# Kernel tuning notes

Hardware: AMD Instinct MI355X
Metric: run time of the kernel (lower is better)

## Reference

```python
import jax, jax.numpy as jnp
import numpy as np

GRID = 8          # proto_grid
EPS = 1e-4        # safe_norm eps
TAU = 20.0        # temperature used throughout


def avg_pool(x, k):
    # non-overlapping avg pool, kernel k divides H and W exactly
    S, C, H, W = x.shape
    return x.reshape(S, C, H // k, k, W // k, k).mean(axis=(3, 5))


def safe_norm(x, axis):
    n = jnp.sqrt(jnp.sum(x * x, axis=axis, keepdims=True))
    return x / jnp.maximum(n, EPS)


def setup_inputs() -> dict:
    key = jax.random.key(0)
    k1, k2, k3 = jax.random.split(key, 3)
    qry = jax.random.normal(k1, (1, 1, 256, 128, 128), dtype=jnp.float32)
    sup_x = jax.random.normal(k2, (1, 5, 1, 256, 128, 128), dtype=jnp.float32)
    sup_y = jax.random.uniform(k3, (1, 5, 1, 128, 128), dtype=jnp.float32)
    return {"qry": qry, "sup_x": sup_x, "sup_y": sup_y, "thresh": 0}


def reference(qry, sup_x, sup_y, thresh):
    # mode == 'gridconv', use_cross_attn=False, isval=False
    qry = qry[:, 0]          # squeeze(1)        -> [1, 256, 128, 128]
    sup_x = sup_x[0, :, 0]   # squeeze(0,2)      -> [5, 256, 128, 128]
    sup_y = sup_y[0]         # squeeze(0)        -> [5, 1, 128, 128]

    shot, nc, H, W = sup_x.shape
    k = H // GRID

    # grid prototypes: avgpool then [shot, nc, g*g] -> [shot, g*g, nc] -> [shot*g*g, nc]
    n_sup = avg_pool(sup_x, k)
    protos = n_sup.reshape(shot, nc, -1).transpose(0, 2, 1).reshape(-1, nc)
    # selection mask: avg_pool(sup_y) > thresh. sup_y is uniform(0,1) and
    # thresh=0, so every grid cell is selected -> selection is the identity
    # (fixed-shape, jit-safe; matches the torch boolean index exactly here).

    # mean-center then safe L2-normalize (channel dim)
    protos = protos - protos.mean(axis=-1, keepdims=True)
    qryc = qry - qry.mean(axis=1, keepdims=True)
    pro_n = safe_norm(protos, axis=1)        # [npro, nc]
    qry_n = safe_norm(qryc, axis=1)          # [b, nc, h, w]

    # 1x1 conv as cosine similarity against prototype bank
    dists = jnp.einsum('bchw,pc->bphw', qry_n, pro_n) * TAU   # [b, npro, h, w]
    prob = jax.nn.softmax(dists, axis=1)
    # bmm combine: channel-wise weighted prototypes per pixel
    ch_proto = jnp.einsum('pc,bphw->bchw', pro_n, prob)       # [b, nc, h, w]
    pred_grid = jnp.sum(qry_n * ch_proto * TAU, axis=1, keepdims=True)

    debug_assign = jnp.argmax(dists, axis=1).astype(jnp.float32)
    return pred_grid, debug_assign
```

## Files before the change

### kernel.cpp

```cpp
#include <hip/hip_runtime.h>

#define NCH   256
#define NPROT 320
#define HW    16384
#define TAU   20.0f
#define EPSN  1e-4f

typedef _Float16 half8 __attribute__((ext_vector_type(8)));
typedef float    f32x4 __attribute__((ext_vector_type(4)));

__global__ __launch_bounds__(256) void k_pool(const float* __restrict__ sup_x,
                                              float* __restrict__ praw) {
    int b = blockIdx.x;
    int t = threadIdx.x;
    const float4* plane = (const float4*)(sup_x + (size_t)b * HW);
    float rsum[8];
    #pragma unroll
    for (int r = 0; r < 8; ++r) rsum[r] = 0.f;
    #pragma unroll
    for (int i = 0; i < 16; ++i) {
        float4 v = plane[i * 256 + t];
        rsum[i >> 1] += v.x + v.y + v.z + v.w;
    }
    __shared__ float part[8][256];
    #pragma unroll
    for (int r = 0; r < 8; ++r) part[r][t] = rsum[r];
    __syncthreads();
    int R  = t >> 5;
    int cw = t & 31;
    float s = 0.f;
    #pragma unroll
    for (int a = 0; a < 8; ++a) s += part[R][a * 32 + cw];
    s += __shfl_xor(s, 1);
    s += __shfl_xor(s, 2);
    if ((t & 3) == 0) {
        int shot = b >> 8, c = b & 255;
        int p = shot * 64 + R * 8 + (cw >> 2);
        praw[(size_t)p * NCH + c] = s * (1.0f / 256.0f);
    }
}

__device__ __forceinline__ float block_sum256(float x, float* ws4, int t) {
    #pragma unroll
    for (int o = 1; o < 64; o <<= 1) x += __shfl_xor(x, o);
    if ((t & 63) == 0) ws4[t >> 6] = x;
    __syncthreads();
    float r = ws4[0] + ws4[1] + ws4[2] + ws4[3];
    __syncthreads();
    return r;
}

__global__ __launch_bounds__(256) void k_norm(const float* __restrict__ praw,
                                              _Float16* __restrict__ PTh,
                                              _Float16* __restrict__ PTl,
                                              float* __restrict__ sp) {
    int p = blockIdx.x;
    int c = threadIdx.x;
    __shared__ float ws4[4];
    float v = praw[p * NCH + c];
    float mean = block_sum256(v, ws4, c) * (1.0f / 256.0f);
    float cen = v - mean;
    float n2 = block_sum256(cen * cen, ws4, c);
    float inv = 1.0f / fmaxf(sqrtf(n2), EPSN);
    float pn = cen * inv;
    _Float16 hi = (_Float16)pn;
    float lo = (pn - (float)hi) * 2048.0f;
    size_t idx = ((size_t)(c >> 3) * NPROT + p) * 8 + (c & 7);
    PTh[idx] = hi;
    PTl[idx] = (_Float16)lo;
    float ssum = block_sum256(pn, ws4, c);
    if (c == 0) sp[p] = ssum;
}

__global__ __launch_bounds__(256, 4) void k_main(const float* __restrict__ qry,
                                                 const _Float16* __restrict__ PTh,
                                                 const _Float16* __restrict__ PTl,
                                                 float* __restrict__ out) {
    __shared__ __align__(16) _Float16 Ah[16 * 256];
    __shared__ __align__(16) _Float16 Al[16 * 256];
    __shared__ __align__(16) float red1[64 * 16];
    __shared__ __align__(16) float red2[64 * 16];
    __shared__ float meanv[16], invnv[16];
    __shared__ float Mw[4][16], Sw[4][16], Tw[4][16], Iw[4][16];
    int t = threadIdx.x;
    int bid = blockIdx.x;
    int tile = (bid & 7) * 128 + (bid >> 3);
    int pixbase = tile * 16;

    int f4 = t & 3;
    int c0 = t >> 2;
    float qv[4][4];
    {
        float ps1[4] = {0.f, 0.f, 0.f, 0.f};
        float ps2[4] = {0.f, 0.f, 0.f, 0.f};
        #pragma unroll
        for (int i = 0; i < 4; ++i) {
            int c = c0 + 64 * i;
            float4 v = *(const float4*)(qry + (size_t)c * HW + pixbase + f4 * 4);
            qv[i][0] = v.x; qv[i][1] = v.y; qv[i][2] = v.z; qv[i][3] = v.w;
            ps1[0] += v.x; ps2[0] = fmaf(v.x, v.x, ps2[0]);
            ps1[1] += v.y; ps2[1] = fmaf(v.y, v.y, ps2[1]);
            ps1[2] += v.z; ps2[2] = fmaf(v.z, v.z, ps2[2]);
            ps1[3] += v.w; ps2[3] = fmaf(v.w, v.w, ps2[3]);
        }
        *(float4*)&red1[c0 * 16 + f4 * 4] = *(float4*)ps1;
        *(float4*)&red2[c0 * 16 + f4 * 4] = *(float4*)ps2;
    }
    __syncthreads();
    if (t < 16) {
        float s1 = 0.f, s2 = 0.f;
        #pragma unroll
        for (int j = 0; j < 64; ++j) { s1 += red1[j * 16 + t]; s2 += red2[j * 16 + t]; }
        float mean = s1 * (1.0f / 256.0f);
        float n2 = fmaxf(s2 - s1 * mean, 0.f);
        meanv[t] = mean;
        invnv[t] = 1.0f / fmaxf(sqrtf(n2), EPSN);
    }
    __syncthreads();

    {
        char* AhB = (char*)Ah;
        char* AlB = (char*)Al;
        #pragma unroll
        for (int j = 0; j < 4; ++j) {
            int px = f4 * 4 + j;
            float mean = meanv[px], invn = invnv[px];
            #pragma unroll
            for (int i = 0; i < 4; ++i) {
                int c = c0 + 64 * i;
                float qn = (qv[i][j] - mean) * invn;
                _Float16 h = (_Float16)qn;
                _Float16 l = (_Float16)((qn - (float)h) * 2048.0f);
                int off = px * 512 + ((2 * c) ^ ((px & 7) << 4));
                *(_Float16*)(AhB + off) = h;
                *(_Float16*)(AlB + off) = l;
            }
        }
    }
    __syncthreads();

    int lane = t & 63, w = t >> 6;
    int col = lane & 15, g4 = lane >> 4;
    int aswz = (col & 7) << 4;
    const char* AhB = (const char*)Ah + col * 512;
    const char* AlB = (const char*)Al + col * 512;
    const half8* BH = (const half8*)PTh;
    const half8* BL = (const half8*)PTl;
    int nb0 = w * 80 + col;

    f32x4 dva[5];
    {
        half8 pbh[6], pbl[6];
        #pragma unroll
        for (int s = 0; s < 6; ++s) {
            int nt = s >> 3, kb = s & 7;
            int idx = (kb * 4 + g4) * 320 + nb0 + nt * 16;
            pbh[s] = BH[idx];
            pbl[s] = BL[idx];
        }
        f32x4 a1 = {0.f, 0.f, 0.f, 0.f};
        f32x4 a2 = {0.f, 0.f, 0.f, 0.f};
        #pragma unroll
        for (int s = 0; s < 40; ++s) {
            int nt = s >> 3, kb = s & 7;
            int buf = s % 6;
            half8 bh = pbh[buf], bl = pbl[buf];
            if (s + 6 < 40) {
                int nt6 = (s + 6) >> 3, kb6 = (s + 6) & 7;
                int idx6 = (kb6 * 4 + g4) * 320 + nb0 + nt6 * 16;
                pbh[buf] = BH[idx6];
                pbl[buf] = BL[idx6];
            }
            int koff = (kb * 64 + g4 * 16) ^ aswz;
            half8 ah = *(const half8*)(AhB + koff);
            half8 al = *(const half8*)(AlB + koff);
            a1 = __builtin_amdgcn_mfma_f32_16x16x32_f16(ah, bh, a1, 0, 0, 0);
            a2 = __builtin_amdgcn_mfma_f32_16x16x32_f16(ah, bl, a2, 0, 0, 0);
            a2 = __builtin_amdgcn_mfma_f32_16x16x32_f16(al, bh, a2, 0, 0, 0);
            if (kb == 7) {
                dva[nt] = a1 + a2 * (1.0f / 2048.0f);
                a1 = (f32x4){0.f, 0.f, 0.f, 0.f};
                a2 = (f32x4){0.f, 0.f, 0.f, 0.f};
            }
        }
    }

    #pragma unroll
    for (int r = 0; r < 4; ++r) {
        int pixel = g4 * 4 + r;
        float dv[5];
        #pragma unroll
        for (int nt = 0; nt < 5; ++nt) dv[nt] = TAU * dva[nt][r];
        float gm = dv[0];
        float gi = (float)(w * 80 + col);
        #pragma unroll
        for (int nt = 1; nt < 5; ++nt)
            if (dv[nt] > gm) { gm = dv[nt]; gi = (float)(w * 80 + nt * 16 + col); }
        #pragma unroll
        for (int o = 1; o < 16; o <<= 1) {
            float om = __shfl_xor(gm, o);
            float oi = __shfl_xor(gi, o);
            if (om > gm || (om == gm && oi < gi)) { gm = om; gi = oi; }
        }
        float S = 0.f, T = 0.f;
        #pragma unroll
        for (int nt = 0; nt < 5; ++nt) {
            float e = __expf(dv[nt] - gm);
            S += e;
            T = fmaf(e, dv[nt], T);
        }
        #pragma unroll
        for (int o = 1; o < 16; o <<= 1) { S += __shfl_xor(S, o); T += __shfl_xor(T, o); }
        if (col == 0) { Mw[w][pixel] = gm; Sw[w][pixel] = S; Tw[w][pixel] = T; Iw[w][pixel] = gi; }
    }
    __syncthreads();

    if (t < 16) {
        float gm = Mw[0][t], gi = Iw[0][t];
        #pragma unroll
        for (int k = 1; k < 4; ++k)
            if (Mw[k][t] > gm) { gm = Mw[k][t]; gi = Iw[k][t]; }
        float S = 0.f, T = 0.f;
        #pragma unroll
        for (int k = 0; k < 4; ++k) {
            float sc = __expf(Mw[k][t] - gm);
            S = fmaf(Sw[k][t], sc, S);
            T = fmaf(Tw[k][t], sc, T);
        }
        out[pixbase + t] = T / S;
        out[HW + pixbase + t] = gi;
    }
}

extern "C" void kernel_launch(void* const* d_in, const int* in_sizes, int n_in,
                              void* d_out, int out_size, void* d_ws, size_t ws_size,
                              hipStream_t stream) {
    const float* qry   = (const float*)d_in[0];
    const float* sup_x = (const float*)d_in[1];
    float* out = (float*)d_out;

    float* praw   = (float*)d_ws;
    _Float16* PTh = (_Float16*)(praw + NPROT * NCH);
    _Float16* PTl = PTh + NPROT * NCH;
    float* sp     = (float*)(PTl + NPROT * NCH);

    k_pool<<<5 * 256, 256, 0, stream>>>(sup_x, praw);
    k_norm<<<NPROT, 256, 0, stream>>>(praw, PTh, PTl, sp);
    k_main<<<HW / 16, 256, 0, stream>>>(qry, PTh, PTl, out);
}
```

Baseline: 156.9 us.

## Process 32 pixels per block to reuse prototype fragments across two M-tiles

Each block in the main kernel now handles 32 query pixels instead of 16. Every prototype B-fragment loaded from global memory feeds two MFMA M-tiles, which halves the total prototype traffic and doubles the MFMA work per load. In exchange the block uses twice the LDS and more registers (extra accumulators, 32 qry values per thread), and launch bounds drop from 4 to 2 blocks per CU. The grid is also halved to 512 blocks, which lowers occupancy and parallelism on a GPU with many CUs.

Result: no change. 159.0 us (+1.3%).

```diff
diff --git a/kernel.cpp b/kernel.cpp
--- a/kernel.cpp
+++ b/kernel.cpp
@@ -72,30 +72,30 @@
     if (c == 0) sp[p] = ssum;
 }
 
-__global__ __launch_bounds__(256, 4) void k_main(const float* __restrict__ qry,
+__global__ __launch_bounds__(256, 2) void k_main(const float* __restrict__ qry,
                                                  const _Float16* __restrict__ PTh,
                                                  const _Float16* __restrict__ PTl,
                                                  float* __restrict__ out) {
-    __shared__ __align__(16) _Float16 Ah[16 * 256];
-    __shared__ __align__(16) _Float16 Al[16 * 256];
-    __shared__ __align__(16) float red1[64 * 16];
-    __shared__ __align__(16) float red2[64 * 16];
-    __shared__ float meanv[16], invnv[16];
-    __shared__ float Mw[4][16], Sw[4][16], Tw[4][16], Iw[4][16];
+    __shared__ __align__(16) _Float16 Ah[32 * 256];
+    __shared__ __align__(16) _Float16 Al[32 * 256];
+    __shared__ __align__(16) float red1[32 * 33];
+    __shared__ __align__(16) float red2[32 * 33];
+    __shared__ float meanv[32], invnv[32];
+    __shared__ float Mw[4][32], Sw[4][32], Tw[4][32], Iw[4][32];
     int t = threadIdx.x;
     int bid = blockIdx.x;
-    int tile = (bid & 7) * 128 + (bid >> 3);
-    int pixbase = tile * 16;
-
-    int f4 = t & 3;
-    int c0 = t >> 2;
-    float qv[4][4];
+    int tile = (bid & 7) * 64 + (bid >> 3);
+    int pixbase = tile * 32;
+
+    int f4 = t & 7;
+    int c0 = t >> 3;
+    float qv[8][4];
     {
         float ps1[4] = {0.f, 0.f, 0.f, 0.f};
         float ps2[4] = {0.f, 0.f, 0.f, 0.f};
         #pragma unroll
-        for (int i = 0; i < 4; ++i) {
-            int c = c0 + 64 * i;
+        for (int i = 0; i < 8; ++i) {
+            int c = c0 + 32 * i;
             float4 v = *(const float4*)(qry + (size_t)c * HW + pixbase + f4 * 4);
             qv[i][0] = v.x; qv[i][1] = v.y; qv[i][2] = v.z; qv[i][3] = v.w;
             ps1[0] += v.x; ps2[0] = fmaf(v.x, v.x, ps2[0]);
@@ -103,14 +103,14 @@
             ps1[2] += v.z; ps2[2] = fmaf(v.z, v.z, ps2[2]);
             ps1[3] += v.w; ps2[3] = fmaf(v.w, v.w, ps2[3]);
         }
-        *(float4*)&red1[c0 * 16 + f4 * 4] = *(float4*)ps1;
-        *(float4*)&red2[c0 * 16 + f4 * 4] = *(float4*)ps2;
-    }
-    __syncthreads();
-    if (t < 16) {
+        *(float4*)&red1[c0 * 33 + f4 * 4] = *(float4*)ps1;
+        *(float4*)&red2[c0 * 33 + f4 * 4] = *(float4*)ps2;
+    }
+    __syncthreads();
+    if (t < 32) {
         float s1 = 0.f, s2 = 0.f;
         #pragma unroll
-        for (int j = 0; j < 64; ++j) { s1 += red1[j * 16 + t]; s2 += red2[j * 16 + t]; }
+        for (int j = 0; j < 32; ++j) { s1 += red1[j * 33 + t]; s2 += red2[j * 33 + t]; }
         float mean = s1 * (1.0f / 256.0f);
         float n2 = fmaxf(s2 - s1 * mean, 0.f);
         meanv[t] = mean;
@@ -126,8 +126,8 @@
             int px = f4 * 4 + j;
             float mean = meanv[px], invn = invnv[px];
             #pragma unroll
-            for (int i = 0; i < 4; ++i) {
-                int c = c0 + 64 * i;
+            for (int i = 0; i < 8; ++i) {
+                int c = c0 + 32 * i;
                 float qn = (qv[i][j] - mean) * invn;
                 _Float16 h = (_Float16)qn;
                 _Float16 l = (_Float16)((qn - (float)h) * 2048.0f);
@@ -148,7 +148,7 @@
     const half8* BL = (const half8*)PTl;
     int nb0 = w * 80 + col;
 
-    f32x4 dva[5];
+    f32x4 dva[2][5];
     {
         half8 pbh[6], pbl[6];
         #pragma unroll
@@ -158,8 +158,8 @@
             pbh[s] = BH[idx];
             pbl[s] = BL[idx];
         }
-        f32x4 a1 = {0.f, 0.f, 0.f, 0.f};
-        f32x4 a2 = {0.f, 0.f, 0.f, 0.f};
+        f32x4 a1_0 = {0.f, 0.f, 0.f, 0.f}, a1_1 = {0.f, 0.f, 0.f, 0.f};
+        f32x4 a2_0 = {0.f, 0.f, 0.f, 0.f}, a2_1 = {0.f, 0.f, 0.f, 0.f};
         #pragma unroll
         for (int s = 0; s < 40; ++s) {
             int nt = s >> 3, kb = s & 7;
@@ -172,50 +172,61 @@
                 pbl[buf] = BL[idx6];
             }
             int koff = (kb * 64 + g4 * 16) ^ aswz;
-            half8 ah = *(const half8*)(AhB + koff);
-            half8 al = *(const half8*)(AlB + koff);
-            a1 = __builtin_amdgcn_mfma_f32_16x16x32_f16(ah, bh, a1, 0, 0, 0);
-            a2 = __builtin_amdgcn_mfma_f32_16x16x32_f16(ah, bl, a2, 0, 0, 0);
-            a2 = __builtin_amdgcn_mfma_f32_16x16x32_f16(al, bh, a2, 0, 0, 0);
+            half8 ah0 = *(const half8*)(AhB + koff);
+            half8 ah1 = *(const half8*)(AhB + koff + 8192);
+            half8 al0 = *(const half8*)(AlB + koff);
+            half8 al1 = *(const half8*)(AlB + koff + 8192);
+            a1_0 = __builtin_amdgcn_mfma_f32_16x16x32_f16(ah0, bh, a1_0, 0, 0, 0);
+            a1_1 = __builtin_amdgcn_mfma_f32_16x16x32_f16(ah1, bh, a1_1, 0, 0, 0);
+            a2_0 = __builtin_amdgcn_mfma_f32_16x16x32_f16(ah0, bl, a2_0, 0, 0, 0);
+            a2_0 = __builtin_amdgcn_mfma_f32_16x16x32_f16(al0, bh, a2_0, 0, 0, 0);
+            a2_1 = __builtin_amdgcn_mfma_f32_16x16x32_f16(ah1, bl, a2_1, 0, 0, 0);
+            a2_1 = __builtin_amdgcn_mfma_f32_16x16x32_f16(al1, bh, a2_1, 0, 0, 0);
             if (kb == 7) {
-                dva[nt] = a1 + a2 * (1.0f / 2048.0f);
-                a1 = (f32x4){0.f, 0.f, 0.f, 0.f};
-                a2 = (f32x4){0.f, 0.f, 0.f, 0.f};
-            }
-        }
-    }
-
-    #pragma unroll
-    for (int r = 0; r < 4; ++r) {
-        int pixel = g4 * 4 + r;
-        float dv[5];
-        #pragma unroll
-        for (int nt = 0; nt < 5; ++nt) dv[nt] = TAU * dva[nt][r];
-        float gm = dv[0];
-        float gi = (float)(w * 80 + col);
-        #pragma unroll
-        for (int nt = 1; nt < 5; ++nt)
-            if (dv[nt] > gm) { gm = dv[nt]; gi = (float)(w * 80 + nt * 16 + col); }
-        #pragma unroll
-        for (int o = 1; o < 16; o <<= 1) {
-            float om = __shfl_xor(gm, o);
-            float oi = __shfl_xor(gi, o);
-            if (om > gm || (om == gm && oi < gi)) { gm = om; gi = oi; }
-        }
-        float S = 0.f, T = 0.f;
-        #pragma unroll
-        for (int nt = 0; nt < 5; ++nt) {
-            float e = __expf(dv[nt] - gm);
-            S += e;
-            T = fmaf(e, dv[nt], T);
-        }
-        #pragma unroll
-        for (int o = 1; o < 16; o <<= 1) { S += __shfl_xor(S, o); T += __shfl_xor(T, o); }
-        if (col == 0) { Mw[w][pixel] = gm; Sw[w][pixel] = S; Tw[w][pixel] = T; Iw[w][pixel] = gi; }
-    }
-    __syncthreads();
-
-    if (t < 16) {
+                dva[0][nt] = a1_0 + a2_0 * (1.0f / 2048.0f);
+                dva[1][nt] = a1_1 + a2_1 * (1.0f / 2048.0f);
+                a1_0 = (f32x4){0.f, 0.f, 0.f, 0.f};
+                a1_1 = (f32x4){0.f, 0.f, 0.f, 0.f};
+                a2_0 = (f32x4){0.f, 0.f, 0.f, 0.f};
+                a2_1 = (f32x4){0.f, 0.f, 0.f, 0.f};
+            }
+        }
+    }
+
+    #pragma unroll
+    for (int mt = 0; mt < 2; ++mt) {
+        #pragma unroll
+        for (int r = 0; r < 4; ++r) {
+            int pixel = mt * 16 + g4 * 4 + r;
+            float dv[5];
+            #pragma unroll
+            for (int nt = 0; nt < 5; ++nt) dv[nt] = TAU * dva[mt][nt][r];
+            float gm = dv[0];
+            float gi = (float)(w * 80 + col);
+            #pragma unroll
+            for (int nt = 1; nt < 5; ++nt)
+                if (dv[nt] > gm) { gm = dv[nt]; gi = (float)(w * 80 + nt * 16 + col); }
+            #pragma unroll
+            for (int o = 1; o < 16; o <<= 1) {
+                float om = __shfl_xor(gm, o);
+                float oi = __shfl_xor(gi, o);
+                if (om > gm || (om == gm && oi < gi)) { gm = om; gi = oi; }
+            }
+            float S = 0.f, T = 0.f;
+            #pragma unroll
+            for (int nt = 0; nt < 5; ++nt) {
+                float e = __expf(dv[nt] - gm);
+                S += e;
+                T = fmaf(e, dv[nt], T);
+            }
+            #pragma unroll
+            for (int o = 1; o < 16; o <<= 1) { S += __shfl_xor(S, o); T += __shfl_xor(T, o); }
+            if (col == 0) { Mw[w][pixel] = gm; Sw[w][pixel] = S; Tw[w][pixel] = T; Iw[w][pixel] = gi; }
+        }
+    }
+    __syncthreads();
+
+    if (t < 32) {
         float gm = Mw[0][t], gi = Iw[0][t];
         #pragma unroll
         for (int k = 1; k < 4; ++k)
@@ -246,5 +257,5 @@
 
     k_pool<<<5 * 256, 256, 0, stream>>>(sup_x, praw);
     k_norm<<<NPROT, 256, 0, stream>>>(praw, PTh, PTl, sp);
-    k_main<<<HW / 16, 256, 0, stream>>>(qry, PTh, PTl, out);
-}
+    k_main<<<HW / 32, 256, 0, stream>>>(qry, PTh, PTl, out);
+}
```
